# Kernel tuning notes

Hardware: AMD Instinct MI355X
Metric: run time of the kernel (lower is better)

## Reference

```python
import jax, jax.numpy as jnp
import numpy as np

EPS = 1e-5
QB = 127.0  # int8 activation quantization bound

def rmsnorm(x):
    # SimpleRMSNorm: x / rms(x), no learned scale
    return x * jax.lax.rsqrt(jnp.mean(x * x, axis=-1, keepdims=True) + EPS)

def activation_quant(x):
    # per-token absmax int8 quant-dequant
    scale = QB / jnp.clip(jnp.max(jnp.abs(x), axis=-1, keepdims=True), EPS)
    return jnp.clip(jnp.round(x * scale), -QB - 1, QB) / scale

def weight_quant(w):
    # per-tensor ternary quant-dequant (BitNet b1.58)
    scale = 1.0 / jnp.clip(jnp.mean(jnp.abs(w)), EPS)
    return jnp.clip(jnp.round(w * scale), -1.0, 1.0) / scale

def ste(x, q):
    # straight-through estimator: forward uses q, gradient flows to x
    return x + jax.lax.stop_gradient(q - x)

def bitlinear(x, w, b):
    xn = rmsnorm(x)
    xq = ste(xn, activation_quant(xn))
    wq = ste(w, weight_quant(w))
    # x: [b, s, d_in], w: [d_out, d_in] -> [b, s, d_out]
    return jnp.einsum('bsd,od->bso', xq, wq) + b

def setup_inputs() -> dict:
    key = jax.random.key(0)
    k1, k2, k3, k4, k5 = jax.random.split(key, 5)
    dim, inner = 1024, 4096
    x = jax.random.normal(k1, (4, 4096, dim), dtype=jnp.float32)
    w1 = jax.random.normal(k2, (inner, dim), dtype=jnp.float32) * (dim ** -0.5)
    b1 = jax.random.normal(k3, (inner,), dtype=jnp.float32) * 0.02
    w2 = jax.random.normal(k4, (dim, inner), dtype=jnp.float32) * (inner ** -0.5)
    b2 = jax.random.normal(k5, (dim,), dtype=jnp.float32) * 0.02
    return {"x": x, "w1": w1, "b1": b1, "w2": w2, "b2": b2}

def reference(x, w1, b1, w2, b2):
    h = jax.nn.gelu(bitlinear(x, w1, b1), approximate=False)  # torch nn.GELU default = exact erf
    # dropout p=0.0 is identity; post_act_ln disabled
    return bitlinear(h, w2, b2)
```

## Files before the change

kernel.cpp:

```cpp
#include <hip/hip_runtime.h>

#define TOK   16384
#define DIM   1024
#define INNER 4096
#define EPSF  1e-5f

typedef int v4i  __attribute__((ext_vector_type(4)));
typedef int v16i __attribute__((ext_vector_type(16)));

static __device__ __forceinline__ void async_copy16(const char* g, char* l) {
    __builtin_amdgcn_global_load_lds(
        (const __attribute__((address_space(1))) unsigned int*)g,
        (__attribute__((address_space(3))) unsigned int*)l, 16, 0, 0);
}

static __device__ __forceinline__ float bf2f(unsigned short u) {
    return __uint_as_float(((unsigned)u) << 16);
}
static __device__ __forceinline__ unsigned short f2bf(float f) {
    unsigned u = __float_as_uint(f);
    return (unsigned short)((u + 0x7fffu + ((u >> 16) & 1u)) >> 16);
}

static __device__ __forceinline__ float fast_erf(float z) {
    float az = fabsf(z);
    float tt = __builtin_amdgcn_rcpf(1.f + 0.3275911f * az);
    float poly = ((((1.061405429f * tt - 1.453152027f) * tt + 1.421413741f) * tt
                   - 0.284496736f) * tt + 0.254829592f) * tt;
    float er = 1.f - poly * __expf(-az * az);
    return copysignf(er, z);
}
static __device__ __forceinline__ float gelu_exact(float v) {
    return 0.5f * v * (1.f + fast_erf(v * 0.70710678118654752f));
}

static __device__ __forceinline__ float waveSum(float v) {
#pragma unroll
    for (int o = 32; o > 0; o >>= 1) v += __shfl_down(v, o, 64);
    return v;
}
static __device__ __forceinline__ float waveMax(float v) {
#pragma unroll
    for (int o = 32; o > 0; o >>= 1) v = fmaxf(v, __shfl_down(v, o, 64));
    return v;
}

__global__ void absmean_k(const float* __restrict__ w, int n4, float* __restrict__ acc) {
    int idx = blockIdx.x * blockDim.x + threadIdx.x;
    int stride = gridDim.x * blockDim.x;
    const float4* w4 = (const float4*)w;
    float s = 0.f;
    for (int i = idx; i < n4; i += stride) {
        float4 v = w4[i];
        s += fabsf(v.x) + fabsf(v.y) + fabsf(v.z) + fabsf(v.w);
    }
    __shared__ float sp[4];
    int wv = threadIdx.x >> 6, lane = threadIdx.x & 63;
    s = waveSum(s);
    if (lane == 0) sp[wv] = s;
    __syncthreads();
    if (threadIdx.x == 0) atomicAdd(acc, sp[0] + sp[1] + sp[2] + sp[3]);
}

__global__ void wquant_k(const float* __restrict__ w, int n,
                         const float* __restrict__ acc, float* __restrict__ wscale,
                         char* __restrict__ wq) {
    float mean = *acc / (float)n;
    float cl = fmaxf(mean, EPSF);
    float s = 1.f / cl;
    if (blockIdx.x == 0 && threadIdx.x == 0) *wscale = cl;
    int idx = blockIdx.x * blockDim.x + threadIdx.x;
    int stride = gridDim.x * blockDim.x;
    int n4 = n >> 2;
    const float4* w4 = (const float4*)w;
    unsigned* q4 = (unsigned*)wq;
    for (int i = idx; i < n4; i += stride) {
        float4 v = w4[i];
        float e[4] = {v.x, v.y, v.z, v.w};
        unsigned packed = 0;
#pragma unroll
        for (int j = 0; j < 4; j++) {
            float r = rintf(e[j] * s);
            r = fminf(fmaxf(r, -1.f), 1.f);
            packed |= ((unsigned)((int)r & 0xff)) << (8 * j);
        }
        q4[i] = packed;
    }
}

template <int D, int VPT>
__global__ void actquant_f32_k(const float* __restrict__ X, char* __restrict__ Q,
                               float* __restrict__ rs_out) {
    int token = blockIdx.x;
    int t = threadIdx.x;
    const float4* xp = (const float4*)(X + (long)token * D);
    float vals[VPT];
    float ss = 0.f, am = 0.f;
#pragma unroll
    for (int j = 0; j < VPT / 4; j++) {
        float4 v = xp[t * (VPT / 4) + j];
        vals[4 * j] = v.x; vals[4 * j + 1] = v.y; vals[4 * j + 2] = v.z; vals[4 * j + 3] = v.w;
        ss += v.x * v.x + v.y * v.y + v.z * v.z + v.w * v.w;
        am = fmaxf(am, fmaxf(fmaxf(fabsf(v.x), fabsf(v.y)), fmaxf(fabsf(v.z), fabsf(v.w))));
    }
    __shared__ float sp[8];
    __shared__ float bc[2];
    int wv = t >> 6, lane = t & 63;
    float S = waveSum(ss);
    float M = waveMax(am);
    if (lane == 0) { sp[wv] = S; sp[4 + wv] = M; }
    __syncthreads();
    if (t == 0) {
        float Sa = sp[0] + sp[1] + sp[2] + sp[3];
        float Ma = fmaxf(fmaxf(sp[4], sp[5]), fmaxf(sp[6], sp[7]));
        float rinv = rsqrtf(Sa * (1.f / (float)D) + EPSF);
        float amn = Ma * rinv;
        float scale = 127.f / fmaxf(amn, EPSF);
        rs_out[token] = 1.f / scale;
        bc[0] = rinv; bc[1] = scale;
    }
    __syncthreads();
    float rinv = bc[0], scale = bc[1];
    unsigned outw[VPT / 4];
#pragma unroll
    for (int j = 0; j < VPT; j++) {
        float r = rintf((vals[j] * rinv) * scale);
        r = fminf(fmaxf(r, -128.f), 127.f);
        unsigned qi = (unsigned)((int)r & 0xff) << (8 * (j & 3));
        if ((j & 3) == 0) outw[j / 4] = qi; else outw[j / 4] |= qi;
    }
    unsigned* qp = (unsigned*)(Q + (long)token * D);
#pragma unroll
    for (int j = 0; j < VPT / 4; j++) qp[t * (VPT / 4) + j] = outw[j];
}

template <int D, int VPT>
__global__ void actquant_bf16_k(const unsigned short* __restrict__ X, char* __restrict__ Q,
                                float* __restrict__ rs_out) {
    int token = blockIdx.x;
    int t = threadIdx.x;
    const uint4* xp = (const uint4*)(X + (long)token * D);
    float vals[VPT];
    float ss = 0.f, am = 0.f;
#pragma unroll
    for (int j = 0; j < VPT / 8; j++) {
        uint4 v = xp[t * (VPT / 8) + j];
        unsigned ws[4] = {v.x, v.y, v.z, v.w};
#pragma unroll
        for (int p = 0; p < 4; p++) {
            float f0 = gelu_exact(bf2f((unsigned short)(ws[p] & 0xffff)));
            float f1 = gelu_exact(bf2f((unsigned short)(ws[p] >> 16)));
            vals[8 * j + 2 * p] = f0; vals[8 * j + 2 * p + 1] = f1;
            ss += f0 * f0 + f1 * f1;
            am = fmaxf(am, fmaxf(fabsf(f0), fabsf(f1)));
        }
    }
    __shared__ float sp[8];
    __shared__ float bc[2];
    int wv = t >> 6, lane = t & 63;
    float S = waveSum(ss);
    float M = waveMax(am);
    if (lane == 0) { sp[wv] = S; sp[4 + wv] = M; }
    __syncthreads();
    if (t == 0) {
        float Sa = sp[0] + sp[1] + sp[2] + sp[3];
        float Ma = fmaxf(fmaxf(sp[4], sp[5]), fmaxf(sp[6], sp[7]));
        float rinv = rsqrtf(Sa * (1.f / (float)D) + EPSF);
        float amn = Ma * rinv;
        float scale = 127.f / fmaxf(amn, EPSF);
        rs_out[token] = 1.f / scale;
        bc[0] = rinv; bc[1] = scale;
    }
    __syncthreads();
    float rinv = bc[0], scale = bc[1];
    unsigned outw[4];
#pragma unroll
    for (int j = 0; j < VPT; j++) {
        float r = rintf((vals[j] * rinv) * scale);
        r = fminf(fmaxf(r, -128.f), 127.f);
        unsigned qi = (unsigned)((int)r & 0xff) << (8 * (j & 3));
        if ((j & 3) == 0) outw[j / 4] = qi; else outw[j / 4] |= qi;
    }
    uint4* qp = (uint4*)(Q + (long)token * D);
    qp[t] = make_uint4(outw[0], outw[1], outw[2], outw[3]);
}

template <int OUT_F32>
__global__ __launch_bounds__(256, 2) void gemm4_k(
    const char* __restrict__ A, const char* __restrict__ Bw,
    const float* __restrict__ rs, const float* __restrict__ wscale_p,
    const float* __restrict__ bias, void* __restrict__ outp,
    int M, int N, int K) {
    __shared__ char L[49152];
    int t = threadIdx.x;
    int lane = t & 63, wv = t >> 6;
    int l31 = lane & 31, kh = lane >> 5;
    int wmi = wv >> 1, wni = wv & 1;

    int gx = gridDim.x;
    int nwg = gx * gridDim.y;
    int bid = blockIdx.y * gx + blockIdx.x;
    int swz = (bid & 7) * (nwg >> 3) + (bid >> 3);
    int bx = swz % gx, by = swz / gx;
    int m0 = by * 256, n0 = bx * 128;

    const char* srcA = A  + (long)(m0 + wv * 16 + (lane & 15)) * K + ((lane >> 4) * 16);
    const char* srcB = Bw + (long)(n0 + wv * 16 + (lane & 15)) * K + ((lane >> 4) * 16);
    char* dstA = L + wv * 1024 + lane * 16;
    char* dstB = L + 32768 + wv * 1024 + lane * 16;

    auto stA = [&](int Tt, int q) {
        async_copy16(srcA + (long)q * 64 * K + ((long)Tt << 6),
                     dstA + (Tt & 1) * 16384 + q * 4096);
    };
    auto stB = [&](int Tt, int q) {
        async_copy16(srcB + (long)q * 64 * K + ((long)Tt << 6),
                     dstB + (Tt & 1) * 8192 + q * 4096);
    };

    int offA[4], offB[2];
#pragma unroll
    for (int i = 0; i < 4; i++) {
        int r = wmi * 128 + i * 32 + l31;
        offA[i] = (r >> 4) * 1024 + (r & 15) * 16 + kh * 256;
    }
#pragma unroll
    for (int j = 0; j < 2; j++) {
        int r = wni * 64 + j * 32 + l31;
        offB[j] = (r >> 4) * 1024 + (r & 15) * 16 + kh * 256;
    }

    v16i acc[4][2] = {};
    int nK = K >> 6;

    stA(0, 0); stA(0, 1); stA(0, 2); stA(0, 3); stB(0, 0); stB(0, 1);
    asm volatile("s_waitcnt vmcnt(0)" ::: "memory");
    asm volatile("s_barrier" ::: "memory");

    for (int T = 0; T < nK; ++T) {
        const char* pA = L + (T & 1) * 16384;
        const char* pB = L + 32768 + (T & 1) * 8192;
        bool pre = (T + 1 < nK);
#pragma unroll
        for (int ks = 0; ks < 2; ++ks) {
            v4i a0 = *(const v4i*)(pA + offA[0] + ks * 512);
            v4i a1 = *(const v4i*)(pA + offA[1] + ks * 512);
            v4i a2 = *(const v4i*)(pA + offA[2] + ks * 512);
            v4i a3 = *(const v4i*)(pA + offA[3] + ks * 512);
            v4i b0 = *(const v4i*)(pB + offB[0] + ks * 512);
            v4i b1 = *(const v4i*)(pB + offB[1] + ks * 512);
            if (pre) {
                if (ks == 0) { stA(T + 1, 0); stA(T + 1, 1); stB(T + 1, 0); }
                else         { stA(T + 1, 2); stA(T + 1, 3); stB(T + 1, 1); }
            }
            __builtin_amdgcn_s_setprio(1);
            acc[0][0] = __builtin_amdgcn_mfma_i32_32x32x32_i8(a0, b0, acc[0][0], 0, 0, 0);
            acc[0][1] = __builtin_amdgcn_mfma_i32_32x32x32_i8(a0, b1, acc[0][1], 0, 0, 0);
            acc[1][0] = __builtin_amdgcn_mfma_i32_32x32x32_i8(a1, b0, acc[1][0], 0, 0, 0);
            acc[1][1] = __builtin_amdgcn_mfma_i32_32x32x32_i8(a1, b1, acc[1][1], 0, 0, 0);
            acc[2][0] = __builtin_amdgcn_mfma_i32_32x32x32_i8(a2, b0, acc[2][0], 0, 0, 0);
            acc[2][1] = __builtin_amdgcn_mfma_i32_32x32x32_i8(a2, b1, acc[2][1], 0, 0, 0);
            acc[3][0] = __builtin_amdgcn_mfma_i32_32x32x32_i8(a3, b0, acc[3][0], 0, 0, 0);
            acc[3][1] = __builtin_amdgcn_mfma_i32_32x32x32_i8(a3, b1, acc[3][1], 0, 0, 0);
            __builtin_amdgcn_s_setprio(0);
        }
        asm volatile("s_waitcnt vmcnt(0)" ::: "memory");
        asm volatile("s_barrier" ::: "memory");
    }

    float wsc = *wscale_p;
    float bv[2];
#pragma unroll
    for (int j = 0; j < 2; j++) bv[j] = bias[n0 + wni * 64 + j * 32 + l31];
#pragma unroll
    for (int i = 0; i < 4; i++) {
        int mbase = m0 + wmi * 128 + i * 32 + 4 * kh;
        float fsv[16];
#pragma unroll
        for (int rg = 0; rg < 16; rg++)
            fsv[rg] = rs[mbase + (rg & 3) + 8 * (rg >> 2)] * wsc;
#pragma unroll
        for (int j = 0; j < 2; j++) {
            int ng = n0 + wni * 64 + j * 32 + l31;
#pragma unroll
            for (int rg = 0; rg < 16; rg++) {
                int mg = mbase + (rg & 3) + 8 * (rg >> 2);
                float v = (float)acc[i][j][rg] * fsv[rg] + bv[j];
                long idx = (long)mg * N + ng;
                if (OUT_F32) ((float*)outp)[idx] = v;
                else ((unsigned short*)outp)[idx] = f2bf(v);
            }
        }
    }
}

extern "C" void kernel_launch(void* const* d_in, const int* in_sizes, int n_in,
                              void* d_out, int out_size, void* d_ws, size_t ws_size,
                              hipStream_t stream) {
    const float* x  = (const float*)d_in[0];
    const float* w1 = (const float*)d_in[1];
    const float* b1 = (const float*)d_in[2];
    const float* w2 = (const float*)d_in[3];
    const float* b2 = (const float*)d_in[4];
    float* out = (float*)d_out;

    char* ws = (char*)d_ws;
    float* acc1 = (float*)(ws + 0);
    float* acc2 = (float*)(ws + 4);
    float* wsc1 = (float*)(ws + 8);
    float* wsc2 = (float*)(ws + 12);
    size_t off = 256;
    char* w1q = ws + off; off += (size_t)INNER * DIM;
    char* w2q = ws + off; off += (size_t)INNER * DIM;
    char* xq1 = ws + off; off += (size_t)TOK * DIM;
    float* rs1 = (float*)(ws + off); off += (size_t)TOK * 4;
    char* xq2 = ws + off; off += (size_t)TOK * INNER;
    float* rs2 = (float*)(ws + off); off += (size_t)TOK * 4;
    unsigned short* h = (unsigned short*)(ws + off);

    hipMemsetAsync(d_ws, 0, 16, stream);

    int nw = INNER * DIM;
    absmean_k<<<1024, 256, 0, stream>>>(w1, nw / 4, acc1);
    absmean_k<<<1024, 256, 0, stream>>>(w2, nw / 4, acc2);
    wquant_k<<<2048, 256, 0, stream>>>(w1, nw, acc1, wsc1, w1q);
    wquant_k<<<2048, 256, 0, stream>>>(w2, nw, acc2, wsc2, w2q);

    actquant_f32_k<DIM, 4><<<TOK, 256, 0, stream>>>(x, xq1, rs1);
    gemm4_k<0><<<dim3(INNER / 128, TOK / 256), 256, 0, stream>>>(
        xq1, w1q, rs1, wsc1, b1, (void*)h, TOK, INNER, DIM);
    actquant_bf16_k<INNER, 16><<<TOK, 256, 0, stream>>>(h, xq2, rs2);
    gemm4_k<1><<<dim3(DIM / 128, TOK / 256), 256, 0, stream>>>(
        xq2, w2q, rs2, wsc2, b2, (void*)out, TOK, DIM, INNER);
}
```

Measured before the change: 438.6 us.

## Enlarge int8 GEMM tile to 256x256 with eight waves and K-step 128

The int8 MFMA GEMM now uses 512-thread workgroups covering a 256x256 output tile. Each iteration stages a 128-deep K slice into 128 KB of double-buffered LDS, and each wave still computes a 128x64 sub-tile. The aim is higher operand reuse per byte loaded, fewer workgroups, and fewer main-loop iterations. In exchange it adds a barrier before and after every MFMA sub-step, and the large LDS footprint limits residency to about one workgroup per CU, which can reduce latency hiding.

```diff
diff --git a/kernel.cpp b/kernel.cpp
--- a/kernel.cpp
+++ b/kernel.cpp
@@ -186,73 +186,81 @@
 }
 
 template <int OUT_F32>
-__global__ __launch_bounds__(256, 2) void gemm4_k(
+__global__ __launch_bounds__(512, 2) void gemm8p_k(
     const char* __restrict__ A, const char* __restrict__ Bw,
     const float* __restrict__ rs, const float* __restrict__ wscale_p,
     const float* __restrict__ bias, void* __restrict__ outp,
     int M, int N, int K) {
-    __shared__ char L[49152];
+    __shared__ char L[131072];
     int t = threadIdx.x;
     int lane = t & 63, wv = t >> 6;
     int l31 = lane & 31, kh = lane >> 5;
-    int wmi = wv >> 1, wni = wv & 1;
+    int wmi = wv >> 2, wni = wv & 3;
 
     int gx = gridDim.x;
     int nwg = gx * gridDim.y;
     int bid = blockIdx.y * gx + blockIdx.x;
     int swz = (bid & 7) * (nwg >> 3) + (bid >> 3);
     int bx = swz % gx, by = swz / gx;
-    int m0 = by * 256, n0 = bx * 128;
-
-    const char* srcA = A  + (long)(m0 + wv * 16 + (lane & 15)) * K + ((lane >> 4) * 16);
-    const char* srcB = Bw + (long)(n0 + wv * 16 + (lane & 15)) * K + ((lane >> 4) * 16);
-    char* dstA = L + wv * 1024 + lane * 16;
-    char* dstB = L + 32768 + wv * 1024 + lane * 16;
-
-    auto stA = [&](int Tt, int q) {
-        async_copy16(srcA + (long)q * 64 * K + ((long)Tt << 6),
-                     dstA + (Tt & 1) * 16384 + q * 4096);
+    int m0 = by * 256, n0 = bx * 256;
+
+    const char* srcA = A  + (long)(m0 + (lane & 15)) * K + ((lane >> 4) * 16);
+    const char* srcB = Bw + (long)(n0 + (lane & 15)) * K + ((lane >> 4) * 16);
+    char* dstA = L + lane * 16;
+    char* dstB = L + 65536 + lane * 16;
+    int sA = wv, sB = wv + 8;
+
+    auto stA = [&](int Tt, int kb, int s) {
+        async_copy16(srcA + (long)(s * 16) * K + kb * 64 + ((long)Tt << 7),
+                     dstA + (Tt & 1) * 32768 + kb * 16384 + s * 1024);
     };
-    auto stB = [&](int Tt, int q) {
-        async_copy16(srcB + (long)q * 64 * K + ((long)Tt << 6),
-                     dstB + (Tt & 1) * 8192 + q * 4096);
+    auto stB = [&](int Tt, int kb, int s) {
+        async_copy16(srcB + (long)(s * 16) * K + kb * 64 + ((long)Tt << 7),
+                     dstB + (Tt & 1) * 32768 + kb * 16384 + s * 1024);
     };
 
-    int offA[4], offB[2];
+    int rA4[4], rB2[2];
 #pragma unroll
     for (int i = 0; i < 4; i++) {
         int r = wmi * 128 + i * 32 + l31;
-        offA[i] = (r >> 4) * 1024 + (r & 15) * 16 + kh * 256;
+        rA4[i] = (r >> 4) * 1024 + (r & 15) * 16;
     }
 #pragma unroll
     for (int j = 0; j < 2; j++) {
         int r = wni * 64 + j * 32 + l31;
-        offB[j] = (r >> 4) * 1024 + (r & 15) * 16 + kh * 256;
-    }
+        rB2[j] = (r >> 4) * 1024 + (r & 15) * 16;
+    }
+    int khoff = kh * 256;
 
     v16i acc[4][2] = {};
-    int nK = K >> 6;
-
-    stA(0, 0); stA(0, 1); stA(0, 2); stA(0, 3); stB(0, 0); stB(0, 1);
+    int nK = K >> 7;
+
+    stA(0, 0, sA); stA(0, 0, sB); stB(0, 0, sA); stB(0, 0, sB);
+    stA(0, 1, sA); stA(0, 1, sB); stB(0, 1, sA); stB(0, 1, sB);
     asm volatile("s_waitcnt vmcnt(0)" ::: "memory");
     asm volatile("s_barrier" ::: "memory");
 
     for (int T = 0; T < nK; ++T) {
-        const char* pA = L + (T & 1) * 16384;
-        const char* pB = L + 32768 + (T & 1) * 8192;
+        int bo = (T & 1) * 32768;
         bool pre = (T + 1 < nK);
 #pragma unroll
-        for (int ks = 0; ks < 2; ++ks) {
-            v4i a0 = *(const v4i*)(pA + offA[0] + ks * 512);
-            v4i a1 = *(const v4i*)(pA + offA[1] + ks * 512);
-            v4i a2 = *(const v4i*)(pA + offA[2] + ks * 512);
-            v4i a3 = *(const v4i*)(pA + offA[3] + ks * 512);
-            v4i b0 = *(const v4i*)(pB + offB[0] + ks * 512);
-            v4i b1 = *(const v4i*)(pB + offB[1] + ks * 512);
+        for (int ks = 0; ks < 4; ++ks) {
+            int so = (ks >> 1) * 16384 + (ks & 1) * 512 + khoff;
+            const char* pA = L + bo + so;
+            const char* pB = L + 65536 + bo + so;
+            v4i a0 = *(const v4i*)(pA + rA4[0]);
+            v4i a1 = *(const v4i*)(pA + rA4[1]);
+            v4i a2 = *(const v4i*)(pA + rA4[2]);
+            v4i a3 = *(const v4i*)(pA + rA4[3]);
+            v4i b0 = *(const v4i*)(pB + rB2[0]);
+            v4i b1 = *(const v4i*)(pB + rB2[1]);
             if (pre) {
-                if (ks == 0) { stA(T + 1, 0); stA(T + 1, 1); stB(T + 1, 0); }
-                else         { stA(T + 1, 2); stA(T + 1, 3); stB(T + 1, 1); }
+                if (ks == 0) { stA(T + 1, 0, sA); stA(T + 1, 0, sB);
+                               stB(T + 1, 0, sA); stB(T + 1, 0, sB); }
+                else if (ks == 1) { stA(T + 1, 1, sA); stA(T + 1, 1, sB);
+                                    stB(T + 1, 1, sA); stB(T + 1, 1, sB); }
             }
+            asm volatile("s_barrier" ::: "memory");
             __builtin_amdgcn_s_setprio(1);
             acc[0][0] = __builtin_amdgcn_mfma_i32_32x32x32_i8(a0, b0, acc[0][0], 0, 0, 0);
             acc[0][1] = __builtin_amdgcn_mfma_i32_32x32x32_i8(a0, b1, acc[0][1], 0, 0, 0);
@@ -263,9 +271,9 @@
             acc[3][0] = __builtin_amdgcn_mfma_i32_32x32x32_i8(a3, b0, acc[3][0], 0, 0, 0);
             acc[3][1] = __builtin_amdgcn_mfma_i32_32x32x32_i8(a3, b1, acc[3][1], 0, 0, 0);
             __builtin_amdgcn_s_setprio(0);
+            if (ks == 3) asm volatile("s_waitcnt vmcnt(0)" ::: "memory");
+            asm volatile("s_barrier" ::: "memory");
         }
-        asm volatile("s_waitcnt vmcnt(0)" ::: "memory");
-        asm volatile("s_barrier" ::: "memory");
     }
 
     float wsc = *wscale_p;
@@ -327,9 +335,9 @@
     wquant_k<<<2048, 256, 0, stream>>>(w2, nw, acc2, wsc2, w2q);
 
     actquant_f32_k<DIM, 4><<<TOK, 256, 0, stream>>>(x, xq1, rs1);
-    gemm4_k<0><<<dim3(INNER / 128, TOK / 256), 256, 0, stream>>>(
+    gemm8p_k<0><<<dim3(INNER / 256, TOK / 256), 512, 0, stream>>>(
         xq1, w1q, rs1, wsc1, b1, (void*)h, TOK, INNER, DIM);
     actquant_bf16_k<INNER, 16><<<TOK, 256, 0, stream>>>(h, xq2, rs2);
-    gemm4_k<1><<<dim3(DIM / 128, TOK / 256), 256, 0, stream>>>(
+    gemm8p_k<1><<<dim3(DIM / 256, TOK / 256), 512, 0, stream>>>(
         xq2, w2q, rs2, wsc2, b2, (void*)out, TOK, DIM, INNER);
 }
```

Measured after the change: 423.7 us. 3.4% less time.
